# Kernel optimization log

Measured on AMD Instinct MI355X. Metric: run time of the kernel, lower is better.

The kernel has to match this reference:

```python
import jax, jax.numpy as jnp
import numpy as np

NUM_SLOTS, SLOT_DIM, FEAT_DIM, HID_DIM = 16, 128, 512, 512
NUM_ITERS, NUM_INIT_ITERS = 2, 3
EPS_ATTN, EPS_LN = 1e-8, 1e-3
SCALE = FEAT_DIM ** -0.5


def _ln(x, g, b):
    mu = jnp.mean(x, axis=-1, keepdims=True)
    var = jnp.mean((x - mu) ** 2, axis=-1, keepdims=True)
    return (x - mu) * jax.lax.rsqrt(var + EPS_LN) * g + b


def setup_inputs() -> dict:
    key = jax.random.key(0)
    ks = jax.random.split(key, 16)
    B, N = 64, 4096
    s = 0.02
    inp = {
        "image_features": jax.random.normal(ks[0], (B, N, FEAT_DIM), jnp.float32),
        "slots": jax.random.normal(ks[1], (B, NUM_SLOTS, SLOT_DIM), jnp.float32),
        "is_first": 1,
        # LayerNorms
        "ln_in_g": jnp.ones((FEAT_DIM,), jnp.float32),
        "ln_in_b": jnp.zeros((FEAT_DIM,), jnp.float32),
        "ln_slot_g": jnp.ones((SLOT_DIM,), jnp.float32),
        "ln_slot_b": jnp.zeros((SLOT_DIM,), jnp.float32),
        "ln_mlp_g": jnp.ones((SLOT_DIM,), jnp.float32),
        "ln_mlp_b": jnp.zeros((SLOT_DIM,), jnp.float32),
        # projections, stored [in, out]
        "Wq": jax.random.normal(ks[2], (SLOT_DIM, SLOT_DIM), jnp.float32) * s,
        "bq": jnp.zeros((SLOT_DIM,), jnp.float32),
        "Wk": jax.random.normal(ks[3], (FEAT_DIM, SLOT_DIM), jnp.float32) * s,
        "bk": jnp.zeros((SLOT_DIM,), jnp.float32),
        "Wv": jax.random.normal(ks[4], (FEAT_DIM, SLOT_DIM), jnp.float32) * s,
        "bv": jnp.zeros((SLOT_DIM,), jnp.float32),
        # GRUCell params (torch layout: [3H, in] / [3H, H], gate order r,z,n)
        "W_ih": jax.random.normal(ks[5], (3 * SLOT_DIM, SLOT_DIM), jnp.float32) * s,
        "W_hh": jax.random.normal(ks[6], (3 * SLOT_DIM, SLOT_DIM), jnp.float32) * s,
        "b_ih": jnp.zeros((3 * SLOT_DIM,), jnp.float32),
        "b_hh": jnp.zeros((3 * SLOT_DIM,), jnp.float32),
        # MLP
        "W1": jax.random.normal(ks[7], (SLOT_DIM, HID_DIM), jnp.float32) * s,
        "b1": jnp.zeros((HID_DIM,), jnp.float32),
        "W2": jax.random.normal(ks[8], (HID_DIM, SLOT_DIM), jnp.float32) * s,
        "b2": jnp.zeros((SLOT_DIM,), jnp.float32),
    }
    return inp


def _gru_cell(x, h, W_ih, W_hh, b_ih, b_hh):
    # torch.nn.GRUCell semantics; x,h: [B*S, H]
    gi = x @ W_ih.T + b_ih  # [BS, 3H]
    gh = h @ W_hh.T + b_hh
    i_r, i_z, i_n = jnp.split(gi, 3, axis=-1)
    h_r, h_z, h_n = jnp.split(gh, 3, axis=-1)
    r = jax.nn.sigmoid(i_r + h_r)
    z = jax.nn.sigmoid(i_z + h_z)
    n = jnp.tanh(i_n + r * h_n)
    return (1.0 - z) * n + z * h


def reference(image_features, slots, is_first,
              ln_in_g, ln_in_b, ln_slot_g, ln_slot_b, ln_mlp_g, ln_mlp_b,
              Wq, bq, Wk, bk, Wv, bv,
              W_ih, W_hh, b_ih, b_hh, W1, b1, W2, b2):
    B = image_features.shape[0]
    feats = _ln(image_features, ln_in_g, ln_in_b)          # [B, N, F]
    k = feats @ Wk + bk                                    # [B, N, D]
    v = feats @ Wv + bv                                    # [B, N, D]
    num_iters = NUM_INIT_ITERS if is_first else NUM_ITERS
    for _ in range(num_iters):
        slots_prev = slots
        q = _ln(slots, ln_slot_g, ln_slot_b) @ Wq + bq     # [B, S, D]
        dots = jnp.einsum('bid,bjd->bij', q, k) * SCALE    # [B, S, N]
        attn = jax.nn.softmax(dots, axis=1) + EPS_ATTN     # softmax over slots
        attn = attn / jnp.sum(attn, axis=-1, keepdims=True)
        updates = jnp.einsum('bij,bjd->bid', attn, v)      # [B, S, D]
        h = _gru_cell(updates.reshape(-1, SLOT_DIM), slots_prev.reshape(-1, SLOT_DIM),
                      W_ih, W_hh, b_ih, b_hh)
        slots = h.reshape(B, -1, SLOT_DIM)
        mlp_out = jax.nn.relu(_ln(slots, ln_mlp_g, ln_mlp_b) @ W1 + b1) @ W2 + b2
        slots = slots + mlp_out
    return slots
```

## Files before the change

kernel.cpp:

```cpp
#include <hip/hip_runtime.h>

typedef __attribute__((ext_vector_type(4))) float f32x4;
typedef __attribute__((ext_vector_type(8))) short bf16x8;
typedef unsigned short u16;

#define LNEPS 1e-3f
#define ATTN_EPS 1e-8f
#define SCALE 0.044194173824159216f

__device__ __forceinline__ u16 f2bf(float f) {
  union { float f; unsigned u; } v; v.f = f;
  unsigned r = v.u + 0x7fffu + ((v.u >> 16) & 1u);
  return (u16)(r >> 16);
}
__device__ __forceinline__ float bf2f(unsigned u) {
  union { float f; unsigned u; } v; v.u = (u & 0xffffu) << 16; return v.f;
}
__device__ __forceinline__ f32x4 mfma16(bf16x8 a, bf16x8 b, f32x4 c) {
  return __builtin_amdgcn_mfma_f32_16x16x32_bf16(a, b, c, 0, 0, 0);
}
__device__ __forceinline__ unsigned pk2(float a, float b) {
  return (unsigned)f2bf(a) | ((unsigned)f2bf(b) << 16);
}

__global__ void cvt_kernel(const float* __restrict__ src, u16* __restrict__ dst,
                           int rows, int cols, int trans) {
  const int total = rows * cols;
  for (int i = blockIdx.x * blockDim.x + threadIdx.x; i < total;
       i += gridDim.x * blockDim.x) {
    const int r = i / cols, c = i - r * cols;
    const u16 v = f2bf(src[i]);
    dst[trans ? (c * rows + r) : i] = v;
  }
}

__global__ void cvt_ktile(const float* __restrict__ src, u16* __restrict__ dst,
                          int coff) {
  const int i = blockIdx.x * blockDim.x + threadIdx.x;
  if (i < 512 * 128) {
    const int k = i >> 7, c = i & 127;
    dst[(k >> 5) * 8192 + (c + coff) * 32 + (k & 31)] = f2bf(src[i]);
  }
}

__global__ __launch_bounds__(256, 5) void k1_lnproj(
    const float* __restrict__ feats, const float* __restrict__ lng,
    const float* __restrict__ lnb, const u16* __restrict__ Wcat,
    const float* __restrict__ bk, const float* __restrict__ bv,
    u16* __restrict__ kbuf, u16* __restrict__ vt) {
  __shared__ alignas(16) union {
    u16 a[32 * 512];
    struct { u16 kq[32 * 136]; float c[128 * 36]; } e;
  } sm;
  const int tid = threadIdx.x;
  const int wave = tid >> 6, lane = tid & 63;
  const int lq = lane >> 4, lm = lane & 15;
  const long long row0 = (long long)blockIdx.x * 32;

  const float4 g0 = *(const float4*)&lng[lane * 8];
  const float4 g1 = *(const float4*)&lng[lane * 8 + 4];
  const float4 bb0 = *(const float4*)&lnb[lane * 8];
  const float4 bb1 = *(const float4*)&lnb[lane * 8 + 4];

  {
    const float* base = feats + (row0 + wave * 8) * 512 + lane * 8;
    float4 x0[8], x1[8];
#pragma unroll
    for (int i = 0; i < 8; ++i) {
      x0[i] = ((const float4*)(base + i * 512))[0];
      x1[i] = ((const float4*)(base + i * 512))[1];
    }
#pragma unroll
    for (int i = 0; i < 8; ++i) {
      const int r = wave * 8 + i;
      float s = (x0[i].x + x0[i].y) + (x0[i].z + x0[i].w) +
                (x1[i].x + x1[i].y) + (x1[i].z + x1[i].w);
      float q = x0[i].x * x0[i].x + x0[i].y * x0[i].y + x0[i].z * x0[i].z +
                x0[i].w * x0[i].w + x1[i].x * x1[i].x + x1[i].y * x1[i].y +
                x1[i].z * x1[i].z + x1[i].w * x1[i].w;
#pragma unroll
      for (int m = 1; m < 64; m <<= 1) {
        s += __shfl_xor(s, m);
        q += __shfl_xor(q, m);
      }
      const float mu = s * (1.f / 512.f);
      const float rstd = rsqrtf(q * (1.f / 512.f) - mu * mu + LNEPS);
      const float y0 = (x0[i].x - mu) * rstd * g0.x + bb0.x;
      const float y1 = (x0[i].y - mu) * rstd * g0.y + bb0.y;
      const float y2 = (x0[i].z - mu) * rstd * g0.z + bb0.z;
      const float y3 = (x0[i].w - mu) * rstd * g0.w + bb0.w;
      const float y4 = (x1[i].x - mu) * rstd * g1.x + bb1.x;
      const float y5 = (x1[i].y - mu) * rstd * g1.y + bb1.y;
      const float y6 = (x1[i].z - mu) * rstd * g1.z + bb1.z;
      const float y7 = (x1[i].w - mu) * rstd * g1.w + bb1.w;
      uint4 w;
      w.x = pk2(y0, y1);
      w.y = pk2(y2, y3);
      w.z = pk2(y4, y5);
      w.w = pk2(y6, y7);
      *(uint4*)((char*)sm.a + r * 1024 + ((lane * 16) ^ ((r & 7) << 4))) = w;
    }
  }
  __syncthreads();

  const int cq = wave;
  f32x4 acc[2][4];
  {
    const f32x4 z4 = {0.f, 0.f, 0.f, 0.f};
#pragma unroll
    for (int m = 0; m < 2; ++m)
#pragma unroll
      for (int n = 0; n < 4; ++n) acc[m][n] = z4;
  }
  const u16* wb = Wcat + (cq * 64 + lm) * 32 + lq * 8;
#pragma unroll 4
  for (int ks = 0; ks < 16; ++ks) {
    bf16x8 a[2], b[4];
#pragma unroll
    for (int mi = 0; mi < 2; ++mi) {
      const int row = mi * 16 + lm;
      a[mi] = *(const bf16x8*)((const char*)sm.a + row * 1024 +
                               ((ks * 64 + lq * 16) ^ ((row & 7) << 4)));
    }
#pragma unroll
    for (int nt = 0; nt < 4; ++nt)
      b[nt] = *(const bf16x8*)&wb[ks * 8192 + nt * 512];
#pragma unroll
    for (int mi = 0; mi < 2; ++mi)
#pragma unroll
      for (int nt = 0; nt < 4; ++nt)
        acc[mi][nt] = mfma16(a[mi], b[nt], acc[mi][nt]);
  }
  __syncthreads();

  if (cq < 2) {
#pragma unroll
    for (int nt = 0; nt < 4; ++nt) {
      const int col = cq * 64 + nt * 16 + lm;
      const float bias = bk[col];
#pragma unroll
      for (int mi = 0; mi < 2; ++mi)
#pragma unroll
        for (int r = 0; r < 4; ++r) {
          const int row = mi * 16 + lq * 4 + r;
          sm.e.kq[row * 136 + col] = f2bf(acc[mi][nt][r] + bias);
        }
    }
  } else {
#pragma unroll
    for (int nt = 0; nt < 4; ++nt) {
      const int d = (cq - 2) * 64 + nt * 16 + lm;
      const float bias = bv[d];
#pragma unroll
      for (int mi = 0; mi < 2; ++mi)
#pragma unroll
        for (int r = 0; r < 4; ++r) {
          const int row = mi * 16 + lq * 4 + r;
          sm.e.c[d * 36 + row] = acc[mi][nt][r] + bias;
        }
    }
  }
  __syncthreads();

  const long long bidx = row0 >> 12;
  const int nbase = (int)(row0 & 4095);
  {
    const int row = tid >> 3, c0 = (tid & 7) * 16;
    const u16* sp = &sm.e.kq[row * 136 + c0];
    u16* dst = kbuf + (row0 + row) * 128 + c0;
    *(uint4*)(dst) = *(const uint4*)(sp);
    *(uint4*)(dst + 8) = *(const uint4*)(sp + 8);
  }
  {
    const int d = tid >> 1, nh = (tid & 1) * 16;
    const float* cp = &sm.e.c[d * 36 + nh];
    u16* dst = vt + (bidx * 128 + d) * 4096 + nbase + nh;
#pragma unroll
    for (int q = 0; q < 2; ++q) {
      uint4 p;
      p.x = pk2(cp[q * 8 + 0], cp[q * 8 + 1]);
      p.y = pk2(cp[q * 8 + 2], cp[q * 8 + 3]);
      p.z = pk2(cp[q * 8 + 4], cp[q * 8 + 5]);
      p.w = pk2(cp[q * 8 + 6], cp[q * 8 + 7]);
      *(uint4*)(dst + q * 8) = p;
    }
  }
}

__global__ __launch_bounds__(256) void k3_attn(
    const float* __restrict__ slots_in, const int* __restrict__ is_first, int iter,
    const float* __restrict__ lsg, const float* __restrict__ lsb,
    const u16* __restrict__ Wqt, const float* __restrict__ bq,
    const u16* __restrict__ kbuf, const u16* __restrict__ vt,
    float* __restrict__ updp, float* __restrict__ rsp) {
  const int ni = (*is_first) ? 3 : 2;
  if (iter >= ni) return;
  __shared__ alignas(16) u16 slns[16 * 136];
  __shared__ alignas(16) u16 qlds[16 * 136];
  __shared__ alignas(16) u16 plds[4][640];
  __shared__ alignas(16) float ures[4][16 * 128];
  __shared__ float rres[4][16];
  const int tid = threadIdx.x;
  const int wave = tid >> 6, lane = tid & 63;
  const int lq = lane >> 4, lm = lane & 15;
  const int b = blockIdx.x >> 3, chunk = blockIdx.x & 7;

  if (wave == 0) {
    const int s = lane >> 2, cc = (lane & 3) * 32;
    const float* sp = slots_in + ((long long)b * 16 + s) * 128 + cc;
    float x[32];
    float sum = 0.f, sq = 0.f;
#pragma unroll
    for (int j = 0; j < 32; ++j) { x[j] = sp[j]; sum += x[j]; sq += x[j] * x[j]; }
    sum += __shfl_xor(sum, 1); sum += __shfl_xor(sum, 2);
    sq  += __shfl_xor(sq, 1);  sq  += __shfl_xor(sq, 2);
    const float mu = sum * (1.f / 128.f);
    const float rstd = rsqrtf(sq * (1.f / 128.f) - mu * mu + LNEPS);
#pragma unroll
    for (int j = 0; j < 32; ++j) {
      const int c = cc + j;
      slns[s * 136 + c] = f2bf((x[j] - mu) * rstd * lsg[c] + lsb[c]);
    }
  }
  __syncthreads();
  {
    f32x4 qa0 = {0.f, 0.f, 0.f, 0.f}, qa1 = {0.f, 0.f, 0.f, 0.f};
#pragma unroll
    for (int ks = 0; ks < 4; ++ks) {
      const bf16x8 af = *(const bf16x8*)&slns[lm * 136 + ks * 32 + lq * 8];
      const bf16x8 b0 = *(const bf16x8*)&Wqt[(wave * 32 + lm) * 128 + ks * 32 + lq * 8];
      const bf16x8 b1 = *(const bf16x8*)&Wqt[(wave * 32 + 16 + lm) * 128 + ks * 32 + lq * 8];
      qa0 = mfma16(af, b0, qa0);
      qa1 = mfma16(af, b1, qa1);
    }
#pragma unroll
    for (int r = 0; r < 4; ++r) {
      const int s = lq * 4 + r;
      const int c0 = wave * 32 + lm, c1 = c0 + 16;
      qlds[s * 136 + c0] = f2bf(qa0[r] + bq[c0]);
      qlds[s * 136 + c1] = f2bf(qa1[r] + bq[c1]);
    }
  }
  __syncthreads();

  bf16x8 qf[4];
#pragma unroll
  for (int ks = 0; ks < 4; ++ks)
    qf[ks] = *(const bf16x8*)&qlds[lm * 136 + ks * 32 + lq * 8];

  float rs0 = 0.f, rs1 = 0.f, rs2 = 0.f, rs3 = 0.f;
  const f32x4 z4 = {0.f, 0.f, 0.f, 0.f};
  f32x4 uacc[8];
#pragma unroll
  for (int i = 0; i < 8; ++i) uacc[i] = z4;
  u16* pw = plds[wave];
  const int n0w = chunk * 512 + wave * 128;
  const u16* kb = kbuf + (long long)b * 4096 * 128;
  const u16* vb = vt + (long long)b * 128 * 4096;

  for (int g = 0; g < 4; ++g) {
    const int nb = n0w + g * 32;
#pragma unroll
    for (int sub = 0; sub < 2; ++sub) {
      f32x4 dot = z4;
      const u16* kr = kb + (long long)(nb + sub * 16 + lm) * 128 + lq * 8;
#pragma unroll
      for (int ks = 0; ks < 4; ++ks)
        dot = mfma16(qf[ks], *(const bf16x8*)&kr[ks * 32], dot);
      const float d0 = dot[0] * SCALE, d1 = dot[1] * SCALE;
      const float d2 = dot[2] * SCALE, d3 = dot[3] * SCALE;
      float m = fmaxf(fmaxf(d0, d1), fmaxf(d2, d3));
      m = fmaxf(m, __shfl_xor(m, 16));
      m = fmaxf(m, __shfl_xor(m, 32));
      const float e0 = __expf(d0 - m), e1 = __expf(d1 - m);
      const float e2 = __expf(d2 - m), e3 = __expf(d3 - m);
      float ss = e0 + e1 + e2 + e3;
      ss += __shfl_xor(ss, 16);
      ss += __shfl_xor(ss, 32);
      const float inv = 1.f / ss;
      const float p0 = e0 * inv + ATTN_EPS, p1 = e1 * inv + ATTN_EPS;
      const float p2 = e2 * inv + ATTN_EPS, p3 = e3 * inv + ATTN_EPS;
      rs0 += p0; rs1 += p1; rs2 += p2; rs3 += p3;
      const int nc = sub * 16 + lm;
      pw[(lq * 4 + 0) * 40 + nc] = f2bf(p0);
      pw[(lq * 4 + 1) * 40 + nc] = f2bf(p1);
      pw[(lq * 4 + 2) * 40 + nc] = f2bf(p2);
      pw[(lq * 4 + 3) * 40 + nc] = f2bf(p3);
    }
    const bf16x8 pa = *(const bf16x8*)&pw[lm * 40 + lq * 8];
    const u16* vr = vb + (long long)lm * 4096 + nb + lq * 8;
#pragma unroll
    for (int dt = 0; dt < 8; ++dt)
      uacc[dt] = mfma16(pa, *(const bf16x8*)&vr[(long long)dt * 16 * 4096], uacc[dt]);
  }
#pragma unroll
  for (int msk = 1; msk < 16; msk <<= 1) {
    rs0 += __shfl_xor(rs0, msk); rs1 += __shfl_xor(rs1, msk);
    rs2 += __shfl_xor(rs2, msk); rs3 += __shfl_xor(rs3, msk);
  }
#pragma unroll
  for (int dt = 0; dt < 8; ++dt)
#pragma unroll
    for (int r = 0; r < 4; ++r)
      ures[wave][(lq * 4 + r) * 128 + dt * 16 + lm] = uacc[dt][r];
  if (lm == 0) {
    rres[wave][lq * 4 + 0] = rs0; rres[wave][lq * 4 + 1] = rs1;
    rres[wave][lq * 4 + 2] = rs2; rres[wave][lq * 4 + 3] = rs3;
  }
  __syncthreads();
  {
    const int e0 = tid * 8;
    float* dst = updp + (long long)(b * 8 + chunk) * 2048 + e0;
#pragma unroll
    for (int e = 0; e < 8; ++e)
      dst[e] = ures[0][e0 + e] + ures[1][e0 + e] + ures[2][e0 + e] + ures[3][e0 + e];
  }
  if (tid < 16)
    rsp[(b * 8 + chunk) * 16 + tid] =
        rres[0][tid] + rres[1][tid] + rres[2][tid] + rres[3][tid];
}

__global__ __launch_bounds__(256) void k4_update(
    const float* __restrict__ slots_in, const int* __restrict__ is_first, int iter,
    const float* __restrict__ updp, const float* __restrict__ rsp,
    const u16* __restrict__ Wih, const u16* __restrict__ Whh,
    const float* __restrict__ bih, const float* __restrict__ bhh,
    const float* __restrict__ lmg, const float* __restrict__ lmb,
    const u16* __restrict__ W1t, const float* __restrict__ b1,
    const u16* __restrict__ W2t, const float* __restrict__ b2,
    float* __restrict__ slots_out, float* __restrict__ dout) {
  const int ni = (*is_first) ? 3 : 2;
  if (iter >= ni) return;
  const bool last = (iter == ni - 1);
  __shared__ float g_ih[16 * 392];
  __shared__ float g_hh[16 * 392];
  __shared__ alignas(16) float hsp[16 * 128];
  __shared__ float rsum[16];
  __shared__ alignas(16) u16 ubf[16 * 136];
  __shared__ alignas(16) u16 xbf[16 * 136];
  __shared__ alignas(16) u16 hidbf[16 * 520];
  const int tid = threadIdx.x;
  const int wave = tid >> 6, lane = tid & 63;
  const int lq = lane >> 4, lm = lane & 15;
  const int b = blockIdx.x;
  const int es = tid >> 4;
  const int ej = (tid & 15) * 8;

  {
    const float* sp = slots_in + (long long)b * 2048 + tid * 8;
    const float4 a = ((const float4*)sp)[0], c = ((const float4*)sp)[1];
    *(float4*)&hsp[tid * 8] = a;
    *(float4*)&hsp[tid * 8 + 4] = c;
    uint4 p;
    p.x = pk2(a.x, a.y);
    p.y = pk2(a.z, a.w);
    p.z = pk2(c.x, c.y);
    p.w = pk2(c.z, c.w);
    *(uint4*)&xbf[es * 136 + ej] = p;
  }
  if (tid < 16) {
    float s = 0.f;
    for (int p = 0; p < 8; ++p) s += rsp[(b * 8 + p) * 16 + tid];
    rsum[tid] = s;
  }
  __syncthreads();
  {
    float acc[8];
#pragma unroll
    for (int e = 0; e < 8; ++e) acc[e] = 0.f;
    for (int p = 0; p < 8; ++p) {
      const float* src = updp + (long long)(b * 8 + p) * 2048 + tid * 8;
      const float4 x = ((const float4*)src)[0], y = ((const float4*)src)[1];
      acc[0] += x.x; acc[1] += x.y; acc[2] += x.z; acc[3] += x.w;
      acc[4] += y.x; acc[5] += y.y; acc[6] += y.z; acc[7] += y.w;
    }
    const float inv = 1.f / rsum[es];
    uint4 p;
    p.x = pk2(acc[0] * inv, acc[1] * inv);
    p.y = pk2(acc[2] * inv, acc[3] * inv);
    p.z = pk2(acc[4] * inv, acc[5] * inv);
    p.w = pk2(acc[6] * inv, acc[7] * inv);
    *(uint4*)&ubf[es * 136 + ej] = p;
  }
  __syncthreads();
  {
    bf16x8 ua[4], ha[4];
#pragma unroll
    for (int ks = 0; ks < 4; ++ks) {
      ua[ks] = *(const bf16x8*)&ubf[lm * 136 + ks * 32 + lq * 8];
      ha[ks] = *(const bf16x8*)&xbf[lm * 136 + ks * 32 + lq * 8];
    }
    const f32x4 z4 = {0.f, 0.f, 0.f, 0.f};
    f32x4 gi[6], gh[6];
#pragma unroll
    for (int t = 0; t < 6; ++t) { gi[t] = z4; gh[t] = z4; }
#pragma unroll
    for (int ks = 0; ks < 4; ++ks)
#pragma unroll
      for (int t = 0; t < 6; ++t) {
        const int col = wave * 96 + t * 16 + lm;
        gi[t] = mfma16(ua[ks], *(const bf16x8*)&Wih[(long long)col * 128 + ks * 32 + lq * 8], gi[t]);
        gh[t] = mfma16(ha[ks], *(const bf16x8*)&Whh[(long long)col * 128 + ks * 32 + lq * 8], gh[t]);
      }
#pragma unroll
    for (int t = 0; t < 6; ++t)
#pragma unroll
      for (int r = 0; r < 4; ++r) {
        const int col = wave * 96 + t * 16 + lm, s = lq * 4 + r;
        g_ih[s * 392 + col] = gi[t][r] + bih[col];
        g_hh[s * 392 + col] = gh[t][r] + bhh[col];
      }
  }
  __syncthreads();
  {
#pragma unroll
    for (int e = 0; e < 8; ++e) {
      const int j = ej + e;
      const float sr = g_ih[es * 392 + j] + g_hh[es * 392 + j];
      const float sz = g_ih[es * 392 + 128 + j] + g_hh[es * 392 + 128 + j];
      const float r = 1.f / (1.f + __expf(-sr));
      const float z = 1.f / (1.f + __expf(-sz));
      const float n = tanhf(g_ih[es * 392 + 256 + j] + r * g_hh[es * 392 + 256 + j]);
      hsp[es * 128 + j] = (1.f - z) * n + z * hsp[es * 128 + j];
    }
  }
  __syncthreads();
  if (wave == 0) {
    const int s = lane >> 2, cc = (lane & 3) * 32;
    float x[32];
    float sum = 0.f, sq = 0.f;
#pragma unroll
    for (int j = 0; j < 32; ++j) {
      x[j] = hsp[s * 128 + cc + j]; sum += x[j]; sq += x[j] * x[j];
    }
    sum += __shfl_xor(sum, 1); sum += __shfl_xor(sum, 2);
    sq  += __shfl_xor(sq, 1);  sq  += __shfl_xor(sq, 2);
    const float mu = sum * (1.f / 128.f);
    const float rstd = rsqrtf(sq * (1.f / 128.f) - mu * mu + LNEPS);
#pragma unroll
    for (int j = 0; j < 32; ++j) {
      const int c = cc + j;
      xbf[s * 136 + c] = f2bf((x[j] - mu) * rstd * lmg[c] + lmb[c]);
    }
  }
  __syncthreads();
  {
    bf16x8 xa[4];
#pragma unroll
    for (int ks = 0; ks < 4; ++ks)
      xa[ks] = *(const bf16x8*)&xbf[lm * 136 + ks * 32 + lq * 8];
    const f32x4 z4 = {0.f, 0.f, 0.f, 0.f};
    f32x4 m1[8];
#pragma unroll
    for (int t = 0; t < 8; ++t) m1[t] = z4;
#pragma unroll
    for (int ks = 0; ks < 4; ++ks)
#pragma unroll
      for (int t = 0; t < 8; ++t) {
        const int col = wave * 128 + t * 16 + lm;
        m1[t] = mfma16(xa[ks], *(const bf16x8*)&W1t[(long long)col * 128 + ks * 32 + lq * 8], m1[t]);
      }
#pragma unroll
    for (int t = 0; t < 8; ++t)
#pragma unroll
      for (int r = 0; r < 4; ++r) {
        const int col = wave * 128 + t * 16 + lm, s = lq * 4 + r;
        hidbf[s * 520 + col] = f2bf(fmaxf(m1[t][r] + b1[col], 0.f));
      }
  }
  __syncthreads();
  {
    const f32x4 z4 = {0.f, 0.f, 0.f, 0.f};
    f32x4 m2a = z4, m2b = z4;
#pragma unroll
    for (int ks = 0; ks < 16; ++ks) {
      const bf16x8 xa = *(const bf16x8*)&hidbf[lm * 520 + ks * 32 + lq * 8];
      m2a = mfma16(xa, *(const bf16x8*)&W2t[(long long)(wave * 32 + lm) * 512 + ks * 32 + lq * 8], m2a);
      m2b = mfma16(xa, *(const bf16x8*)&W2t[(long long)(wave * 32 + 16 + lm) * 512 + ks * 32 + lq * 8], m2b);
    }
#pragma unroll
    for (int r = 0; r < 4; ++r) {
      const int s = lq * 4 + r;
      const int c0 = wave * 32 + lm, c1 = c0 + 16;
      const float o0 = m2a[r] + b2[c0] + hsp[s * 128 + c0];
      const float o1 = m2b[r] + b2[c1] + hsp[s * 128 + c1];
      float* o = slots_out + ((long long)b * 16 + s) * 128;
      o[c0] = o0; o[c1] = o1;
      if (last) {
        float* d = dout + ((long long)b * 16 + s) * 128;
        d[c0] = o0; d[c1] = o1;
      }
    }
  }
}

extern "C" void kernel_launch(void* const* d_in, const int* in_sizes, int n_in,
                              void* d_out, int out_size, void* d_ws, size_t ws_size,
                              hipStream_t stream) {
  (void)in_sizes; (void)n_in; (void)out_size; (void)ws_size;
  const float* feats    = (const float*)d_in[0];
  const float* slots0   = (const float*)d_in[1];
  const int*   is_first = (const int*)d_in[2];
  const float* ln_in_g  = (const float*)d_in[3];
  const float* ln_in_b  = (const float*)d_in[4];
  const float* ln_sl_g  = (const float*)d_in[5];
  const float* ln_sl_b  = (const float*)d_in[6];
  const float* ln_ml_g  = (const float*)d_in[7];
  const float* ln_ml_b  = (const float*)d_in[8];
  const float* Wq  = (const float*)d_in[9];
  const float* bq  = (const float*)d_in[10];
  const float* Wk  = (const float*)d_in[11];
  const float* bk  = (const float*)d_in[12];
  const float* Wv  = (const float*)d_in[13];
  const float* bv  = (const float*)d_in[14];
  const float* Wih_f = (const float*)d_in[15];
  const float* Whh_f = (const float*)d_in[16];
  const float* bih = (const float*)d_in[17];
  const float* bhh = (const float*)d_in[18];
  const float* W1  = (const float*)d_in[19];
  const float* b1  = (const float*)d_in[20];
  const float* W2  = (const float*)d_in[21];
  const float* b2  = (const float*)d_in[22];

  char* ws = (char*)d_ws;
  size_t off = 0;
  auto alloc = [&](size_t bytes) -> void* {
    void* p = ws + off;
    off = (off + bytes + 255) & ~(size_t)255;
    return p;
  };
  u16* kbuf   = (u16*)alloc((size_t)64 * 4096 * 128 * 2);
  u16* vt     = (u16*)alloc((size_t)64 * 4096 * 128 * 2);
  u16* Wcat   = (u16*)alloc((size_t)16 * 256 * 32 * 2);
  u16* Wqt    = (u16*)alloc((size_t)128 * 128 * 2);
  u16* Wih    = (u16*)alloc((size_t)384 * 128 * 2);
  u16* Whh    = (u16*)alloc((size_t)384 * 128 * 2);
  u16* W1t    = (u16*)alloc((size_t)512 * 128 * 2);
  u16* W2t    = (u16*)alloc((size_t)128 * 512 * 2);
  float* updp = (float*)alloc((size_t)64 * 8 * 2048 * 4);
  float* rsp  = (float*)alloc((size_t)64 * 8 * 16 * 4);
  float* slA  = (float*)alloc((size_t)64 * 2048 * 4);
  float* slB  = (float*)alloc((size_t)64 * 2048 * 4);

  cvt_ktile<<<256, 256, 0, stream>>>(Wk, Wcat, 0);
  cvt_ktile<<<256, 256, 0, stream>>>(Wv, Wcat, 128);
  cvt_kernel<<<64, 256, 0, stream>>>(Wq, Wqt, 128, 128, 1);
  cvt_kernel<<<64, 256, 0, stream>>>(Wih_f, Wih, 384, 128, 0);
  cvt_kernel<<<64, 256, 0, stream>>>(Whh_f, Whh, 384, 128, 0);
  cvt_kernel<<<64, 256, 0, stream>>>(W1, W1t, 128, 512, 1);
  cvt_kernel<<<64, 256, 0, stream>>>(W2, W2t, 512, 128, 1);

  k1_lnproj<<<8192, 256, 0, stream>>>(feats, ln_in_g, ln_in_b, Wcat, bk, bv, kbuf, vt);

  float* bufs[2] = {slA, slB};
  for (int it = 0; it < 3; ++it) {
    const float* sin_ = (it == 0) ? slots0 : bufs[(it + 1) & 1];
    float* sout = bufs[it & 1];
    k3_attn<<<512, 256, 0, stream>>>(sin_, is_first, it, ln_sl_g, ln_sl_b, Wqt, bq,
                                     kbuf, vt, updp, rsp);
    k4_update<<<64, 256, 0, stream>>>(sin_, is_first, it, updp, rsp, Wih, Whh,
                                      bih, bhh, ln_ml_g, ln_ml_b, W1t, b1, W2t, b2,
                                      sout, (float*)d_out);
  }
}
```

Before: 413.8 us.

## Split input LayerNorm into standalone kernel and stage bf16 tiles via global_load_lds

Unfuses the input LayerNorm from the K/V projection GEMM. A new streaming kernel writes normalized, swizzled bf16 rows to a global buffer, and the GEMM kernel pulls them into LDS with direct global-to-LDS loads. The aim is to separate the memory-bound normalization from the MFMA projection so each kernel can run at its own occupancy. The cost is an extra 256 MB bf16 round trip through HBM, since it is written once and read back, plus one more kernel launch.

```diff
diff --git a/kernel.cpp b/kernel.cpp
--- a/kernel.cpp
+++ b/kernel.cpp
@@ -21,6 +21,11 @@
 }
 __device__ __forceinline__ unsigned pk2(float a, float b) {
   return (unsigned)f2bf(a) | ((unsigned)f2bf(b) << 16);
+}
+__device__ __forceinline__ void gload_lds16(const void* g, void* l) {
+  __builtin_amdgcn_global_load_lds(
+      (const __attribute__((address_space(1))) void*)g,
+      (__attribute__((address_space(3))) void*)l, 16, 0, 0);
 }
 
 __global__ void cvt_kernel(const float* __restrict__ src, u16* __restrict__ dst,
@@ -43,9 +48,59 @@
   }
 }
 
-__global__ __launch_bounds__(256, 5) void k1_lnproj(
+__global__ __launch_bounds__(256, 4) void k0_lnstream(
     const float* __restrict__ feats, const float* __restrict__ lng,
-    const float* __restrict__ lnb, const u16* __restrict__ Wcat,
+    const float* __restrict__ lnb, u16* __restrict__ xn) {
+  const int wave = threadIdx.x >> 6, lane = threadIdx.x & 63;
+  const long long row0 = (long long)blockIdx.x * 32 + wave * 8;
+
+  const float4 g0 = *(const float4*)&lng[lane * 8];
+  const float4 g1 = *(const float4*)&lng[lane * 8 + 4];
+  const float4 bb0 = *(const float4*)&lnb[lane * 8];
+  const float4 bb1 = *(const float4*)&lnb[lane * 8 + 4];
+
+  const float* base = feats + row0 * 512 + lane * 8;
+  float4 x0[8], x1[8];
+#pragma unroll
+  for (int i = 0; i < 8; ++i) {
+    x0[i] = ((const float4*)(base + i * 512))[0];
+    x1[i] = ((const float4*)(base + i * 512))[1];
+  }
+#pragma unroll
+  for (int i = 0; i < 8; ++i) {
+    const long long grow = row0 + i;
+    float s = (x0[i].x + x0[i].y) + (x0[i].z + x0[i].w) +
+              (x1[i].x + x1[i].y) + (x1[i].z + x1[i].w);
+    float q = x0[i].x * x0[i].x + x0[i].y * x0[i].y + x0[i].z * x0[i].z +
+              x0[i].w * x0[i].w + x1[i].x * x1[i].x + x1[i].y * x1[i].y +
+              x1[i].z * x1[i].z + x1[i].w * x1[i].w;
+#pragma unroll
+    for (int m = 1; m < 64; m <<= 1) {
+      s += __shfl_xor(s, m);
+      q += __shfl_xor(q, m);
+    }
+    const float mu = s * (1.f / 512.f);
+    const float rstd = rsqrtf(q * (1.f / 512.f) - mu * mu + LNEPS);
+    const float y0 = (x0[i].x - mu) * rstd * g0.x + bb0.x;
+    const float y1 = (x0[i].y - mu) * rstd * g0.y + bb0.y;
+    const float y2 = (x0[i].z - mu) * rstd * g0.z + bb0.z;
+    const float y3 = (x0[i].w - mu) * rstd * g0.w + bb0.w;
+    const float y4 = (x1[i].x - mu) * rstd * g1.x + bb1.x;
+    const float y5 = (x1[i].y - mu) * rstd * g1.y + bb1.y;
+    const float y6 = (x1[i].z - mu) * rstd * g1.z + bb1.z;
+    const float y7 = (x1[i].w - mu) * rstd * g1.w + bb1.w;
+    uint4 w;
+    w.x = pk2(y0, y1);
+    w.y = pk2(y2, y3);
+    w.z = pk2(y4, y5);
+    w.w = pk2(y6, y7);
+    *(uint4*)((char*)xn + grow * 1024 +
+              ((lane * 16) ^ (((int)grow & 7) << 4))) = w;
+  }
+}
+
+__global__ __launch_bounds__(256, 5) void k1_gemm(
+    const u16* __restrict__ xn, const u16* __restrict__ Wcat,
     const float* __restrict__ bk, const float* __restrict__ bv,
     u16* __restrict__ kbuf, u16* __restrict__ vt) {
   __shared__ alignas(16) union {
@@ -57,48 +112,12 @@
   const int lq = lane >> 4, lm = lane & 15;
   const long long row0 = (long long)blockIdx.x * 32;
 
-  const float4 g0 = *(const float4*)&lng[lane * 8];
-  const float4 g1 = *(const float4*)&lng[lane * 8 + 4];
-  const float4 bb0 = *(const float4*)&lnb[lane * 8];
-  const float4 bb1 = *(const float4*)&lnb[lane * 8 + 4];
-
-  {
-    const float* base = feats + (row0 + wave * 8) * 512 + lane * 8;
-    float4 x0[8], x1[8];
-#pragma unroll
-    for (int i = 0; i < 8; ++i) {
-      x0[i] = ((const float4*)(base + i * 512))[0];
-      x1[i] = ((const float4*)(base + i * 512))[1];
-    }
-#pragma unroll
-    for (int i = 0; i < 8; ++i) {
-      const int r = wave * 8 + i;
-      float s = (x0[i].x + x0[i].y) + (x0[i].z + x0[i].w) +
-                (x1[i].x + x1[i].y) + (x1[i].z + x1[i].w);
-      float q = x0[i].x * x0[i].x + x0[i].y * x0[i].y + x0[i].z * x0[i].z +
-                x0[i].w * x0[i].w + x1[i].x * x1[i].x + x1[i].y * x1[i].y +
-                x1[i].z * x1[i].z + x1[i].w * x1[i].w;
-#pragma unroll
-      for (int m = 1; m < 64; m <<= 1) {
-        s += __shfl_xor(s, m);
-        q += __shfl_xor(q, m);
-      }
-      const float mu = s * (1.f / 512.f);
-      const float rstd = rsqrtf(q * (1.f / 512.f) - mu * mu + LNEPS);
-      const float y0 = (x0[i].x - mu) * rstd * g0.x + bb0.x;
-      const float y1 = (x0[i].y - mu) * rstd * g0.y + bb0.y;
-      const float y2 = (x0[i].z - mu) * rstd * g0.z + bb0.z;
-      const float y3 = (x0[i].w - mu) * rstd * g0.w + bb0.w;
-      const float y4 = (x1[i].x - mu) * rstd * g1.x + bb1.x;
-      const float y5 = (x1[i].y - mu) * rstd * g1.y + bb1.y;
-      const float y6 = (x1[i].z - mu) * rstd * g1.z + bb1.z;
-      const float y7 = (x1[i].w - mu) * rstd * g1.w + bb1.w;
-      uint4 w;
-      w.x = pk2(y0, y1);
-      w.y = pk2(y2, y3);
-      w.z = pk2(y4, y5);
-      w.w = pk2(y6, y7);
-      *(uint4*)((char*)sm.a + r * 1024 + ((lane * 16) ^ ((r & 7) << 4))) = w;
+  {
+    const char* gsrc = (const char*)xn + row0 * 1024;
+#pragma unroll
+    for (int jj = 0; jj < 8; ++jj) {
+      const int inst = wave * 8 + jj;
+      gload_lds16(gsrc + inst * 1024 + lane * 16, (char*)sm.a + inst * 1024);
     }
   }
   __syncthreads();
@@ -531,6 +550,7 @@
   };
   u16* kbuf   = (u16*)alloc((size_t)64 * 4096 * 128 * 2);
   u16* vt     = (u16*)alloc((size_t)64 * 4096 * 128 * 2);
+  u16* xn     = (u16*)alloc((size_t)64 * 4096 * 512 * 2);
   u16* Wcat   = (u16*)alloc((size_t)16 * 256 * 32 * 2);
   u16* Wqt    = (u16*)alloc((size_t)128 * 128 * 2);
   u16* Wih    = (u16*)alloc((size_t)384 * 128 * 2);
@@ -550,7 +570,8 @@
   cvt_kernel<<<64, 256, 0, stream>>>(W1, W1t, 128, 512, 1);
   cvt_kernel<<<64, 256, 0, stream>>>(W2, W2t, 512, 128, 1);
 
-  k1_lnproj<<<8192, 256, 0, stream>>>(feats, ln_in_g, ln_in_b, Wcat, bk, bv, kbuf, vt);
+  k0_lnstream<<<8192, 256, 0, stream>>>(feats, ln_in_g, ln_in_b, xn);
+  k1_gemm<<<8192, 256, 0, stream>>>(xn, Wcat, bk, bv, kbuf, vt);
 
   float* bufs[2] = {slA, slB};
   for (int it = 0; it < 3; ++it) {
```

Result: slower. 511.9 us (+23.7%).
